# Optimization experiments

Measured on AMD Instinct MI355X. Metric: run time of the kernel, lower is better.

## Reference

```python
import jax, jax.numpy as jnp
import numpy as np

N_QUBITS = 4
N_LAYERS = 2
DIM = 2 ** N_QUBITS
BATCH = 1048576

# --- static circuit structure (wire 0 = most significant bit, pennylane default.qubit convention) ---

def _cnot_perm(c, t, n=N_QUBITS):
    """Index permutation implementing CNOT(control=c, target=t) on a 2^n statevector."""
    idx = np.arange(2 ** n)
    cm = 1 << (n - 1 - c)
    tm = 1 << (n - 1 - t)
    return jnp.asarray(np.where(idx & cm, idx ^ tm, idx))

# PauliZ expectation signs: +1 if bit of wire w is 0, else -1 -> [DIM, N_QUBITS]
_ZSIGNS = jnp.asarray(
    np.array([[1.0 - 2.0 * ((i >> (N_QUBITS - 1 - w)) & 1) for w in range(N_QUBITS)]
              for i in range(DIM)], dtype=np.float32))


def _apply_1q_batched(state, gate, w):
    """Apply per-sample 2x2 gate [B,2,2] to wire w of state [B, DIM]."""
    B = state.shape[0]
    left, right = 2 ** w, 2 ** (N_QUBITS - 1 - w)
    s = state.reshape(B, left, 2, right)
    return jnp.einsum('bij,bljr->blir', gate, s).reshape(B, DIM)


def _apply_1q_shared(state, gate, w):
    """Apply shared 2x2 gate [2,2] to wire w of state [B, DIM]."""
    B = state.shape[0]
    left, right = 2 ** w, 2 ** (N_QUBITS - 1 - w)
    s = state.reshape(B, left, 2, right)
    return jnp.einsum('ij,bljr->blir', gate, s).reshape(B, DIM)


def _ry_gate(theta):
    """RY(theta) for batched theta [B] -> [B,2,2] complex64."""
    c = jnp.cos(theta / 2).astype(jnp.complex64)
    s = jnp.sin(theta / 2).astype(jnp.complex64)
    return jnp.stack([jnp.stack([c, -s], -1), jnp.stack([s, c], -1)], -2)


def _rot_gate(phi, theta, omega):
    """PennyLane Rot(phi, theta, omega) = RZ(omega) RY(theta) RZ(phi) -> [2,2] complex64."""
    c = jnp.cos(theta / 2)
    s = jnp.sin(theta / 2)
    g00 = jnp.exp(-0.5j * (phi + omega)) * c
    g01 = -jnp.exp(0.5j * (phi - omega)) * s
    g10 = jnp.exp(-0.5j * (phi - omega)) * s
    g11 = jnp.exp(0.5j * (phi + omega)) * c
    return jnp.stack([jnp.stack([g00, g01]), jnp.stack([g10, g11])]).astype(jnp.complex64)


def setup_inputs() -> dict:
    key = jax.random.key(0)
    k1, k2 = jax.random.split(key)
    x = jax.random.normal(k1, (BATCH, N_QUBITS), dtype=jnp.float32)
    params = jax.random.normal(k2, (N_LAYERS, N_QUBITS, 3), dtype=jnp.float32) * 0.1
    return {"x": x, "params": params}


def reference(x, params):
    B = x.shape[0]
    # angle encoding: tanh(x) * pi/2
    ang = jnp.tanh(x) * (np.pi / 2)  # [B, n_qubits]

    # initial |0...0> state, batched
    state = jnp.zeros((B, DIM), dtype=jnp.complex64).at[:, 0].set(1.0)

    # data-dependent RY layer
    for w in range(N_QUBITS):
        state = _apply_1q_batched(state, _ry_gate(ang[:, w]), w)

    for layer in range(N_LAYERS):
        # CNOT chain
        for i in range(N_QUBITS - 1):
            state = state[:, _cnot_perm(i, i + 1)]
        # parameterized Rot gates (shared across batch)
        for i in range(N_QUBITS):
            p = params[layer, i]
            state = _apply_1q_shared(state, _rot_gate(p[0], p[1], p[2]), i)
        # ring-closing CNOT
        state = state[:, _cnot_perm(0, N_QUBITS - 1)]

    probs = state.real ** 2 + state.imag ** 2  # [B, DIM] float32
    return probs @ _ZSIGNS  # [B, n_qubits] PauliZ expectations
```

## Files before the change

### kernel.cpp

```cpp
#include <hip/hip_runtime.h>


typedef __attribute__((ext_vector_type(2))) float v2f;

__device__ __forceinline__ float hwsin(float rad) {
  return __builtin_amdgcn_sinf(rad * 0.15915494309189535f);
}
__device__ __forceinline__ float hwcos(float rad) {
  return __builtin_amdgcn_cosf(rad * 0.15915494309189535f);
}

#define TRIGM(xv, U, V) { \
  float e_  = __builtin_amdgcn_exp2f((xv) * 2.8853900817779268f); \
  float th_ = 1.0f - 2.0f * __builtin_amdgcn_rcpf(e_ + 1.0f); \
  U = __builtin_amdgcn_cosf(th_ * 0.25f); \
  V = __builtin_amdgcn_sinf(th_ * 0.25f); }

#define SAMPLE_TRIG_PAIR(P, XA, XB) \
  TRIGM(XA.x, u0_##P.x, v0_##P.x) TRIGM(XA.y, u1_##P.x, v1_##P.x) \
  TRIGM(XA.z, u2_##P.x, v2_##P.x) TRIGM(XA.w, u3_##P.x, v3_##P.x) \
  TRIGM(XB.x, u0_##P.y, v0_##P.y) TRIGM(XB.y, u1_##P.y, v1_##P.y) \
  TRIGM(XB.z, u2_##P.y, v2_##P.y) TRIGM(XB.w, u3_##P.y, v3_##P.y)

#define DECL_TRIG_PAIR(P) \
  v2f u0_##P, v0_##P, u1_##P, v1_##P, u2_##P, v2_##P, u3_##P, v3_##P;

#define ACC3P(P) { \
  v2f t_ = __builtin_elementwise_fma(cz2, v3_##P, \
           __builtin_elementwise_fma(cy2, u3_##P, cx2)); \
  if (e3 == 0) a3_##P = t_; \
  else a3_##P = __builtin_elementwise_fma(t_, (e3 == 1) ? u2_##P : v2_##P, a3_##P); }

#define ACC2P(P) { \
  if (e2 == 0) a2_##P = a3_##P; \
  else a2_##P = __builtin_elementwise_fma(a3_##P, (e2 == 1) ? u1_##P : v1_##P, a2_##P); }

#define ACC1RP(P) { \
  v2f m_ = (e1 == 1) ? u0_##P : v0_##P; \
  a1_##P = (e1 == 0) ? a2_##P : __builtin_elementwise_fma(a2_##P, m_, a1_##P); }

#define ALLP(M) M(01) M(23) M(45) M(67)

__global__ __launch_bounds__(256) void qel_fused(const float4* __restrict__ x4,
                                                 const float* __restrict__ params,
                                                 float4* __restrict__ out4,
                                                 int eighth) {
  __shared__ float2 U2[16][17];
  __shared__ float A[4][16][16];
  __shared__ float S1[4][3][8][8];
  __shared__ float S2[4][3][3][4][4];
  __shared__ float S3[4][3][3][3][2][2];
  __shared__ float4 Cs[108];
  __shared__ float Olds[4][8][256];

  const int tid = threadIdx.x;
  const int gid = blockIdx.x * 256 + tid;
  const bool act = gid < eighth;
  const int g = act ? gid : 0;

  float4 X0 = x4[g];
  float4 X1 = x4[g + eighth];
  float4 X2 = x4[g + 2 * eighth];
  float4 X3 = x4[g + 3 * eighth];
  float4 X4 = x4[g + 4 * eighth];
  float4 X5 = x4[g + 5 * eighth];
  float4 X6 = x4[g + 6 * eighth];
  float4 X7 = x4[g + 7 * eighth];

  {
    const int c = tid >> 4, r = tid & 15;
    float vr = (r == c) ? 1.f : 0.f;
    float vi = 0.f;

    #pragma unroll
    for (int layer = 0; layer < 2; layer++) {
      #pragma unroll
      for (int i = 0; i < 3; i++) {
        const int cm = 8 >> i, tm = 4 >> i;
        float pvr = __shfl_xor(vr, tm);
        float pvi = __shfl_xor(vi, tm);
        vr = (r & cm) ? pvr : vr;
        vi = (r & cm) ? pvi : vi;
      }
      #pragma unroll
      for (int w = 0; w < 4; w++) {
        float phi   = params[layer * 12 + w * 3 + 0];
        float theta = params[layer * 12 + w * 3 + 1];
        float omega = params[layer * 12 + w * 3 + 2];
        float ct = hwcos(theta * 0.5f), st = hwsin(theta * 0.5f);
        float ap = -0.5f * (phi + omega), am = 0.5f * (phi - omega);
        float g00r =  hwcos(ap) * ct, g00i =  hwsin(ap) * ct;
        float g01r = -hwcos(am) * st, g01i = -hwsin(am) * st;
        float g10r =  hwcos(am) * st, g10i = -hwsin(am) * st;
        float g11r =  g00r,           g11i = -g00i;
        const int tm = 8 >> w;
        const bool hi = (r & tm) != 0;
        float pvr = __shfl_xor(vr, tm);
        float pvi = __shfl_xor(vi, tm);
        float o0r = hi ? pvr : vr, o0i = hi ? pvi : vi;
        float o1r = hi ? vr : pvr, o1i = hi ? vi : pvi;
        float gar = hi ? g10r : g00r, gai = hi ? g10i : g00i;
        float gbr = hi ? g11r : g01r, gbi = hi ? g11i : g01i;
        vr = gar * o0r - gai * o0i + gbr * o1r - gbi * o1i;
        vi = gar * o0i + gai * o0r + gbr * o1i + gbi * o1r;
      }
      {
        float pvr = __shfl_xor(vr, 1);
        float pvi = __shfl_xor(vi, 1);
        vr = (r & 8) ? pvr : vr;
        vi = (r & 8) ? pvi : vi;
      }
    }
    U2[c][r] = make_float2(vr, vi);
  }
  __syncthreads();

  {
    const int j = tid >> 4, k = tid & 15;
    float s0 = 0.f, s1 = 0.f, s2 = 0.f, s3 = 0.f;
    #pragma unroll
    for (int i = 0; i < 16; i++) {
      float2 uj = U2[j][i], uk = U2[k][i];
      float p = uj.x * uk.x + uj.y * uk.y;
      s0 += (i & 8) ? -p : p;
      s1 += (i & 4) ? -p : p;
      s2 += (i & 2) ? -p : p;
      s3 += (i & 1) ? -p : p;
    }
    A[0][j][k] = s0; A[1][j][k] = s1; A[2][j][k] = s2; A[3][j][k] = s3;
  }
  __syncthreads();

  {
    const int w = tid >> 6, j = (tid >> 3) & 7, k = tid & 7;
    float x00 = A[w][j][k],     x01 = A[w][j][k + 8];
    float x10 = A[w][j + 8][k], x11 = A[w][j + 8][k + 8];
    S1[w][0][j][k] = 0.5f * (x00 + x11);
    S1[w][1][j][k] = 0.5f * (x00 - x11);
    S1[w][2][j][k] = 0.5f * (x01 + x10);
  }
  __syncthreads();
  if (tid < 192) {
    const int w = tid / 48, r = tid % 48;
    const int f0 = r >> 4, j = (r >> 2) & 3, k = r & 3;
    float x00 = S1[w][f0][j][k],     x01 = S1[w][f0][j][k + 4];
    float x10 = S1[w][f0][j + 4][k], x11 = S1[w][f0][j + 4][k + 4];
    S2[w][f0][0][j][k] = 0.5f * (x00 + x11);
    S2[w][f0][1][j][k] = 0.5f * (x00 - x11);
    S2[w][f0][2][j][k] = 0.5f * (x01 + x10);
  }
  __syncthreads();
  if (tid < 144) {
    const int w = tid / 36, r = tid % 36;
    const int f0 = r / 12, f1 = (r >> 2) % 3, j = (r >> 1) & 1, k = r & 1;
    float x00 = S2[w][f0][f1][j][k],     x01 = S2[w][f0][f1][j][k + 2];
    float x10 = S2[w][f0][f1][j + 2][k], x11 = S2[w][f0][f1][j + 2][k + 2];
    S3[w][f0][f1][0][j][k] = 0.5f * (x00 + x11);
    S3[w][f0][f1][1][j][k] = 0.5f * (x00 - x11);
    S3[w][f0][f1][2][j][k] = 0.5f * (x01 + x10);
  }
  __syncthreads();
  if (tid < 108) {
    const int w = tid / 27, r = tid % 27;
    const int f0 = r / 9, f1 = (r / 3) % 3, f2 = r % 3;
    float y00 = S3[w][f0][f1][f2][0][0], y01 = S3[w][f0][f1][f2][0][1];
    float y10 = S3[w][f0][f1][f2][1][0], y11 = S3[w][f0][f1][f2][1][1];
    float4 o;
    o.x = 0.5f * (y00 + y11);
    o.y = 0.5f * (y00 - y11);
    o.z = 0.5f * (y01 + y10);
    o.w = 0.f;
    Cs[tid] = o;
  }

  ALLP(DECL_TRIG_PAIR)
  SAMPLE_TRIG_PAIR(01, X0, X1)
  SAMPLE_TRIG_PAIR(23, X2, X3)
  SAMPLE_TRIG_PAIR(45, X4, X5)
  SAMPLE_TRIG_PAIR(67, X6, X7)

  __syncthreads();

  #pragma unroll 1
  for (int W = 0; W < 4; W++) {
    v2f a1_01 = {0.f, 0.f}, a1_23 = {0.f, 0.f};
    v2f a1_45 = {0.f, 0.f}, a1_67 = {0.f, 0.f};
    #pragma unroll 1
    for (int e1 = 0; e1 < 3; e1++) {
      const float4* cb = &Cs[W * 27 + e1 * 9];
      v2f a2_01, a2_23, a2_45, a2_67;
      #pragma unroll
      for (int e2 = 0; e2 < 3; e2++) {
        v2f a3_01, a3_23, a3_45, a3_67;
        #pragma unroll
        for (int e3 = 0; e3 < 3; e3++) {
          float4 c = cb[e2 * 3 + e3];
          v2f cx2 = {c.x, c.x}, cy2 = {c.y, c.y}, cz2 = {c.z, c.z};
          ALLP(ACC3P)
        }
        ALLP(ACC2P)
      }
      ALLP(ACC1RP)
    }
    Olds[W][0][tid] = a1_01.x;
    Olds[W][1][tid] = a1_01.y;
    Olds[W][2][tid] = a1_23.x;
    Olds[W][3][tid] = a1_23.y;
    Olds[W][4][tid] = a1_45.x;
    Olds[W][5][tid] = a1_45.y;
    Olds[W][6][tid] = a1_67.x;
    Olds[W][7][tid] = a1_67.y;
  }

  if (act) {
    #pragma unroll
    for (int k = 0; k < 8; k++) {
      out4[gid + k * eighth] = make_float4(Olds[0][k][tid], Olds[1][k][tid],
                                           Olds[2][k][tid], Olds[3][k][tid]);
    }
  }
}


extern "C" void kernel_launch(void* const* d_in, const int* in_sizes, int n_in,
                              void* d_out, int out_size, void* d_ws, size_t ws_size,
                              hipStream_t stream) {
  const float* x      = (const float*)d_in[0];
  const float* params = (const float*)d_in[1];
  float* out = (float*)d_out;

  int B = in_sizes[0] / 4;
  int eighth = B / 8;
  int blocks = (eighth + 255) / 256;

  qel_fused<<<blocks, 256, 0, stream>>>((const float4*)x, params,
                                        (float4*)out, eighth);
}
```

Before: 19.57 us.

## Pack two output wires per lane pair using op_sel v_pk_fma with interleaved coefficients

The packed-FMA tensor contraction is reorganised so that each v2f lane pair holds two output wires (W) of the same sample, not the same wire for two samples. The coefficients are stored interleaved by wire pair in LDS, and the per-sample cos/sin pairs are selected through op_sel in inline-asm v_pk_fma_f32. This removes the scalar broadcasts and the cndmask selects between u and v, and halves the outer W loop trip count. The cost is opaque inline asm that the compiler cannot schedule around, and a different LDS read pattern.

```diff
diff --git a/kernel.cpp b/kernel.cpp
--- a/kernel.cpp
+++ b/kernel.cpp
@@ -16,30 +16,38 @@
   U = __builtin_amdgcn_cosf(th_ * 0.25f); \
   V = __builtin_amdgcn_sinf(th_ * 0.25f); }
 
-#define SAMPLE_TRIG_PAIR(P, XA, XB) \
-  TRIGM(XA.x, u0_##P.x, v0_##P.x) TRIGM(XA.y, u1_##P.x, v1_##P.x) \
-  TRIGM(XA.z, u2_##P.x, v2_##P.x) TRIGM(XA.w, u3_##P.x, v3_##P.x) \
-  TRIGM(XB.x, u0_##P.y, v0_##P.y) TRIGM(XB.y, u1_##P.y, v1_##P.y) \
-  TRIGM(XB.z, u2_##P.y, v2_##P.y) TRIGM(XB.w, u3_##P.y, v3_##P.y)
-
-#define DECL_TRIG_PAIR(P) \
-  v2f u0_##P, v0_##P, u1_##P, v1_##P, u2_##P, v2_##P, u3_##P, v3_##P;
-
-#define ACC3P(P) { \
-  v2f t_ = __builtin_elementwise_fma(cz2, v3_##P, \
-           __builtin_elementwise_fma(cy2, u3_##P, cx2)); \
-  if (e3 == 0) a3_##P = t_; \
-  else a3_##P = __builtin_elementwise_fma(t_, (e3 == 1) ? u2_##P : v2_##P, a3_##P); }
-
-#define ACC2P(P) { \
-  if (e2 == 0) a2_##P = a3_##P; \
-  else a2_##P = __builtin_elementwise_fma(a3_##P, (e2 == 1) ? u1_##P : v1_##P, a2_##P); }
-
-#define ACC1RP(P) { \
-  v2f m_ = (e1 == 1) ? u0_##P : v0_##P; \
-  a1_##P = (e1 == 0) ? a2_##P : __builtin_elementwise_fma(a2_##P, m_, a1_##P); }
-
-#define ALLP(M) M(01) M(23) M(45) M(67)
+#define SAMPLE_TRIG(K, XK) \
+  TRIGM(XK.x, uv0_##K.x, uv0_##K.y) TRIGM(XK.y, uv1_##K.x, uv1_##K.y) \
+  TRIGM(XK.z, uv2_##K.x, uv2_##K.y) TRIGM(XK.w, uv3_##K.x, uv3_##K.y)
+
+#define DECL_TRIG(K) v2f uv0_##K, uv1_##K, uv2_##K, uv3_##K;
+
+#define PKFMA_L(D, A, B, C) \
+  asm("v_pk_fma_f32 %0, %1, %2, %3 op_sel:[0,0,0] op_sel_hi:[1,0,1]" \
+      : "=v"(D) : "v"(A), "v"(B), "v"(C));
+#define PKFMA_H(D, A, B, C) \
+  asm("v_pk_fma_f32 %0, %1, %2, %3 op_sel:[0,1,0] op_sel_hi:[1,1,1]" \
+      : "=v"(D) : "v"(A), "v"(B), "v"(C));
+
+#define PACC3(K) { \
+  v2f t_; \
+  PKFMA_L(t_, cy, uv3_##K, cx) \
+  PKFMA_H(t_, cz, uv3_##K, t_) \
+  if (e3 == 0)      a3_##K = t_; \
+  else if (e3 == 1) { PKFMA_L(a3_##K, t_, uv2_##K, a3_##K) } \
+  else              { PKFMA_H(a3_##K, t_, uv2_##K, a3_##K) } }
+
+#define PACC2(K) { \
+  if (e2 == 0)      a2_##K = a3_##K; \
+  else if (e2 == 1) { PKFMA_L(a2_##K, a3_##K, uv1_##K, a2_##K) } \
+  else              { PKFMA_H(a2_##K, a3_##K, uv1_##K, a2_##K) } }
+
+#define PACC1(K) { \
+  if (e1 == 0)      a1_##K = a2_##K; \
+  else if (e1 == 1) { PKFMA_L(a1_##K, a2_##K, uv0_##K, a1_##K) } \
+  else              { PKFMA_H(a1_##K, a2_##K, uv0_##K, a1_##K) } }
+
+#define ALL8(M) M(0) M(1) M(2) M(3) M(4) M(5) M(6) M(7)
 
 __global__ __launch_bounds__(256) void qel_fused(const float4* __restrict__ x4,
                                                  const float* __restrict__ params,
@@ -50,7 +58,7 @@
   __shared__ float S1[4][3][8][8];
   __shared__ float S2[4][3][3][4][4];
   __shared__ float S3[4][3][3][3][2][2];
-  __shared__ float4 Cs[108];
+  __shared__ v2f CsPk[27 * 3 * 2];
   __shared__ float Olds[4][8][256];
 
   const int tid = threadIdx.x;
@@ -165,51 +173,52 @@
     const int f0 = r / 9, f1 = (r / 3) % 3, f2 = r % 3;
     float y00 = S3[w][f0][f1][f2][0][0], y01 = S3[w][f0][f1][f2][0][1];
     float y10 = S3[w][f0][f1][f2][1][0], y11 = S3[w][f0][f1][f2][1][1];
-    float4 o;
-    o.x = 0.5f * (y00 + y11);
-    o.y = 0.5f * (y00 - y11);
-    o.z = 0.5f * (y01 + y10);
-    o.w = 0.f;
-    Cs[tid] = o;
-  }
-
-  ALLP(DECL_TRIG_PAIR)
-  SAMPLE_TRIG_PAIR(01, X0, X1)
-  SAMPLE_TRIG_PAIR(23, X2, X3)
-  SAMPLE_TRIG_PAIR(45, X4, X5)
-  SAMPLE_TRIG_PAIR(67, X6, X7)
+    float cx = 0.5f * (y00 + y11);
+    float cy = 0.5f * (y00 - y11);
+    float cz = 0.5f * (y01 + y10);
+    float* base = (float*)CsPk;
+    const int wp = w >> 1, h = w & 1;
+    base[((r * 3 + 0) * 2 + wp) * 2 + h] = cx;
+    base[((r * 3 + 1) * 2 + wp) * 2 + h] = cy;
+    base[((r * 3 + 2) * 2 + wp) * 2 + h] = cz;
+  }
+
+  ALL8(DECL_TRIG)
+  SAMPLE_TRIG(0, X0) SAMPLE_TRIG(1, X1) SAMPLE_TRIG(2, X2) SAMPLE_TRIG(3, X3)
+  SAMPLE_TRIG(4, X4) SAMPLE_TRIG(5, X5) SAMPLE_TRIG(6, X6) SAMPLE_TRIG(7, X7)
 
   __syncthreads();
 
   #pragma unroll 1
-  for (int W = 0; W < 4; W++) {
-    v2f a1_01 = {0.f, 0.f}, a1_23 = {0.f, 0.f};
-    v2f a1_45 = {0.f, 0.f}, a1_67 = {0.f, 0.f};
+  for (int wp = 0; wp < 2; wp++) {
+    v2f a1_0, a1_1, a1_2, a1_3, a1_4, a1_5, a1_6, a1_7;
     #pragma unroll 1
     for (int e1 = 0; e1 < 3; e1++) {
-      const float4* cb = &Cs[W * 27 + e1 * 9];
-      v2f a2_01, a2_23, a2_45, a2_67;
+      const v2f* C0 = CsPk + e1 * 54 + wp;
+      v2f a2_0, a2_1, a2_2, a2_3, a2_4, a2_5, a2_6, a2_7;
       #pragma unroll
       for (int e2 = 0; e2 < 3; e2++) {
-        v2f a3_01, a3_23, a3_45, a3_67;
+        v2f a3_0, a3_1, a3_2, a3_3, a3_4, a3_5, a3_6, a3_7;
         #pragma unroll
         for (int e3 = 0; e3 < 3; e3++) {
-          float4 c = cb[e2 * 3 + e3];
-          v2f cx2 = {c.x, c.x}, cy2 = {c.y, c.y}, cz2 = {c.z, c.z};
-          ALLP(ACC3P)
+          const int idx2 = e2 * 3 + e3;
+          v2f cx = C0[idx2 * 6];
+          v2f cy = C0[idx2 * 6 + 2];
+          v2f cz = C0[idx2 * 6 + 4];
+          ALL8(PACC3)
         }
-        ALLP(ACC2P)
-      }
-      ALLP(ACC1RP)
-    }
-    Olds[W][0][tid] = a1_01.x;
-    Olds[W][1][tid] = a1_01.y;
-    Olds[W][2][tid] = a1_23.x;
-    Olds[W][3][tid] = a1_23.y;
-    Olds[W][4][tid] = a1_45.x;
-    Olds[W][5][tid] = a1_45.y;
-    Olds[W][6][tid] = a1_67.x;
-    Olds[W][7][tid] = a1_67.y;
+        ALL8(PACC2)
+      }
+      ALL8(PACC1)
+    }
+    Olds[wp * 2][0][tid] = a1_0.x;     Olds[wp * 2 + 1][0][tid] = a1_0.y;
+    Olds[wp * 2][1][tid] = a1_1.x;     Olds[wp * 2 + 1][1][tid] = a1_1.y;
+    Olds[wp * 2][2][tid] = a1_2.x;     Olds[wp * 2 + 1][2][tid] = a1_2.y;
+    Olds[wp * 2][3][tid] = a1_3.x;     Olds[wp * 2 + 1][3][tid] = a1_3.y;
+    Olds[wp * 2][4][tid] = a1_4.x;     Olds[wp * 2 + 1][4][tid] = a1_4.y;
+    Olds[wp * 2][5][tid] = a1_5.x;     Olds[wp * 2 + 1][5][tid] = a1_5.y;
+    Olds[wp * 2][6][tid] = a1_6.x;     Olds[wp * 2 + 1][6][tid] = a1_6.y;
+    Olds[wp * 2][7][tid] = a1_7.x;     Olds[wp * 2 + 1][7][tid] = a1_7.y;
   }
 
   if (act) {
```

Result: slower. 21.15 us (+8.1%).
